# Performance work log

Measured on AMD Instinct MI355X. Metric: run time of the kernel, lower is better.

Reference implementation:

```python
import jax, jax.numpy as jnp
import numpy as np

B, L, S, H, C = 64, 512, 512, 768, 9  # batch, bert subword len, word seq len, hidden, num_classes


def setup_inputs() -> dict:
    key = jax.random.key(0)
    k1, k2, k3 = jax.random.split(key, 3)
    rng = np.random.RandomState(0)
    # per-word subword counts in {1,2,3}; truncate so totals fit in L subword slots
    lens = rng.randint(1, 4, size=(B, S))
    cum = lens.cumsum(axis=1)
    keep = cum <= L
    ids_lens = (lens * keep).astype(np.int32)
    totals = ids_lens.sum(axis=1)
    attention_mask = (np.arange(L)[None, :] < totals[:, None]).astype(np.int32)
    label_mask = ids_lens > 0
    label_ids = (rng.randint(0, C, size=(B, S)) * label_mask).astype(np.int32)
    bert_out = jax.random.normal(k1, (B, L, H), dtype=jnp.float32)
    W = jax.random.normal(k2, (H, C), dtype=jnp.float32) * 0.02
    b = jnp.zeros((C,), dtype=jnp.float32)
    return {
        "bert_out": bert_out,
        "W": W,
        "b": b,
        "attention_mask": jnp.asarray(attention_mask),
        "ids_lens": jnp.asarray(ids_lens),
        "label_ids": jnp.asarray(label_ids),
        "label_mask": jnp.asarray(label_mask),
    }


def reference(bert_out, W, b, attention_mask, ids_lens, label_ids, label_mask):
    Bv, Lv, Hv = bert_out.shape
    Sv = ids_lens.shape[1]
    nseg = Bv * Sv
    am = attention_mask.astype(jnp.int32)
    # subword position within each example's valid region
    sidx = jnp.cumsum(am, axis=1) - 1                       # [B, L]
    # word index for each subword: searchsorted into cumulative word lengths
    ends = jnp.cumsum(ids_lens, axis=1)                     # [B, S]
    widx = jax.vmap(lambda e, s: jnp.searchsorted(e, s, side='right'))(ends, sidx)
    seg = jnp.where(am > 0, widx + jnp.arange(Bv)[:, None] * Sv, nseg)  # pad bucket = nseg
    flat = bert_out.reshape(Bv * Lv, Hv)
    segf = seg.reshape(Bv * Lv)
    sums = jax.ops.segment_sum(flat, segf, num_segments=nseg + 1)[:nseg]
    cnts = jax.ops.segment_sum(jnp.ones((Bv * Lv,), bert_out.dtype), segf,
                               num_segments=nseg + 1)[:nseg]
    mean = sums / jnp.maximum(cnts, 1.0)[:, None]           # segment mean (split().mean(0))
    word_mask = (ids_lens > 0).reshape(nseg)
    embed = jnp.where(word_mask[:, None], mean, 0.0).reshape(Bv, Sv, Hv)  # masked_scatter
    # dropout in eval mode = identity
    logits = embed @ W + b                                  # [B, S, C]
    logp = jax.nn.log_softmax(logits, axis=-1)
    lab = jnp.clip(label_ids, 0, W.shape[1] - 1)
    nll = -jnp.take_along_axis(logp, lab[..., None].astype(jnp.int32), axis=-1)[..., 0]
    valid = label_mask.astype(bert_out.dtype)
    loss = jnp.sum(nll * valid) / jnp.maximum(jnp.sum(valid), 1.0)
    pred = jnp.argmax(logits, axis=-1)
    return loss, pred
```

## Files before the change

kernel.cpp:

```cpp
#include <hip/hip_runtime.h>

#define BB 64
#define LL 512
#define SS 512
#define HH 768
#define CC 9
#define NROWS (BB * LL)
#define RLS 12
#define G1 1024
#define ROWS_PER_BLOCK 32
#define WPS 64
#define G2 (BB * SS / WPS)

template <int CTRL>
__device__ __forceinline__ float dpp_add(float x) {
    int y = __builtin_amdgcn_update_dpp(0, __float_as_int(x), CTRL, 0xf, 0xf, true);
    return x + __int_as_float(y);
}
__device__ __forceinline__ float rsum64(float x) {
    x = dpp_add<0x111>(x);
    x = dpp_add<0x112>(x);
    x = dpp_add<0x114>(x);
    x = dpp_add<0x118>(x);
    x = dpp_add<0x142>(x);
    x = dpp_add<0x143>(x);
    return x;
}

__global__ __launch_bounds__(256) void wt_kernel(const float* __restrict__ Wm,
                                                 float* __restrict__ WT_g) {
    int e = blockIdx.x * 256 + threadIdx.x;
    if (e < HH * CC) {
        int h = e / CC;
        int c = e - h * CC;
        WT_g[c * HH + h] = Wm[e];
    }
}

__global__ __launch_bounds__(256) void row_gemm_kernel(
    const float* __restrict__ bert,
    const float* __restrict__ WT_g,
    float* __restrict__ RL)
{
    int wave = threadIdx.x >> 6;
    int lane = threadIdx.x & 63;
    int hoff = lane * 4;

    float4 wreg[CC][3];
#pragma unroll
    for (int c = 0; c < CC; c++)
#pragma unroll
        for (int c3 = 0; c3 < 3; c3++)
            wreg[c][c3] = *reinterpret_cast<const float4*>(WT_g + c * HH + c3 * 256 + hoff);

    size_t row0 = (size_t)blockIdx.x * ROWS_PER_BLOCK + wave * 8;

#pragma unroll
    for (int r = 0; r < 8; ++r) {
        const float* p = bert + (row0 + r) * HH + hoff;
        float4 f0 = *reinterpret_cast<const float4*>(p);
        float4 f1 = *reinterpret_cast<const float4*>(p + 256);
        float4 f2 = *reinterpret_cast<const float4*>(p + 512);

        float acc[CC];
#pragma unroll
        for (int c = 0; c < CC; c++) {
            acc[c] = f0.x * wreg[c][0].x + f0.y * wreg[c][0].y
                   + f0.z * wreg[c][0].z + f0.w * wreg[c][0].w
                   + f1.x * wreg[c][1].x + f1.y * wreg[c][1].y
                   + f1.z * wreg[c][1].z + f1.w * wreg[c][1].w
                   + f2.x * wreg[c][2].x + f2.y * wreg[c][2].y
                   + f2.z * wreg[c][2].z + f2.w * wreg[c][2].w;
        }
#pragma unroll
        for (int c = 0; c < CC; c++) acc[c] = rsum64(acc[c]);

        if (lane == 63) {
            float* dst = RL + (row0 + r) * RLS;
            float4 s0; s0.x = acc[0]; s0.y = acc[1]; s0.z = acc[2]; s0.w = acc[3];
            float4 s1; s1.x = acc[4]; s1.y = acc[5]; s1.z = acc[6]; s1.w = acc[7];
            *reinterpret_cast<float4*>(dst) = s0;
            *reinterpret_cast<float4*>(dst + 4) = s1;
            dst[8] = acc[8];
        }
    }
}

__global__ __launch_bounds__(256) void pool_kernel(
    const float* __restrict__ RL,
    const float* __restrict__ bias,
    const int* __restrict__ ids_lens,
    const int* __restrict__ label_ids,
    float* __restrict__ pred_out,
    float* __restrict__ nll_part,
    float* __restrict__ cnt_part)
{
    __shared__ int wlen[WPS], woff[WPS];
    __shared__ float red[4];
    __shared__ int s_start;

    int b = blockIdx.x >> 3;
    int s8 = blockIdx.x & 7;
    int w0 = s8 * WPS;
    const int* lens = ids_lens + b * SS;

    int t = threadIdx.x, lane = t & 63, wave = t >> 6;

    if (t < WPS) wlen[t] = lens[w0 + t];

    int part = 0;
    for (int i = t; i < w0; i += 256) part += lens[i];
    float pf = rsum64((float)part);
    if (lane == 63) red[wave] = pf;
    __syncthreads();
    if (t == 0) {
        int run = 0;
#pragma unroll
        for (int k = 0; k < WPS; k++) { woff[k] = run; run += wlen[k]; }
        s_start = (int)(red[0] + red[1] + red[2] + red[3]);
    }
    __syncthreads();

    if (t < 64) {
        int k = t;
        int len = wlen[k];
        int off = s_start + woff[k];
        const float* base = RL + ((size_t)b * LL + off) * RLS;

        float s[CC];
#pragma unroll
        for (int c = 0; c < CC; c++) s[c] = 0.0f;
        for (int j = 0; j < len; ++j) {
            const float* p = base + j * RLS;
            float4 a = *reinterpret_cast<const float4*>(p);
            float4 c4 = *reinterpret_cast<const float4*>(p + 4);
            s[0] += a.x;  s[1] += a.y;  s[2] += a.z;  s[3] += a.w;
            s[4] += c4.x; s[5] += c4.y; s[6] += c4.z; s[7] += c4.w;
            s[8] += p[8];
        }
        float inv = 1.0f / (float)(len > 0 ? len : 1);
        float lg[CC];
#pragma unroll
        for (int c = 0; c < CC; c++) lg[c] = s[c] * inv + bias[c];

        float mx = lg[0];
        int arg = 0;
#pragma unroll
        for (int c = 1; c < CC; c++) {
            if (lg[c] > mx) { mx = lg[c]; arg = c; }
        }
        float se = 0.0f;
#pragma unroll
        for (int c = 0; c < CC; c++) se += expf(lg[c] - mx);
        float lse = mx + logf(se);

        int g = b * SS + w0 + k;
        int lab = label_ids[g];
        lab = lab < 0 ? 0 : (lab > CC - 1 ? CC - 1 : lab);
        float valid = (len > 0) ? 1.0f : 0.0f;
        float nll = (lse - lg[lab]) * valid;

        pred_out[g] = (float)arg;

        float rn = rsum64(nll);
        float rc = rsum64(valid);
        if (t == 63) {
            nll_part[blockIdx.x] = rn;
            cnt_part[blockIdx.x] = rc;
        }
    }
}

__global__ __launch_bounds__(512) void finalize_kernel(
    const float* __restrict__ nll_part,
    const float* __restrict__ cnt_part,
    float* __restrict__ out_loss) {
    __shared__ float sn[8], sc[8];
    int t = threadIdx.x, lane = t & 63, wave = t >> 6;
    float n = rsum64(nll_part[t]);
    float c = rsum64(cnt_part[t]);
    if (lane == 63) { sn[wave] = n; sc[wave] = c; }
    __syncthreads();
    if (t == 0) {
        float tn = 0.0f, tc = 0.0f;
#pragma unroll
        for (int i = 0; i < 8; i++) { tn += sn[i]; tc += sc[i]; }
        out_loss[0] = tn / fmaxf(tc, 1.0f);
    }
}

extern "C" void kernel_launch(void* const* d_in, const int* in_sizes, int n_in,
                              void* d_out, int out_size, void* d_ws, size_t ws_size,
                              hipStream_t stream) {
    const float* bert = (const float*)d_in[0];
    const float* Wm   = (const float*)d_in[1];
    const float* bias = (const float*)d_in[2];
    const int* ids_lens  = (const int*)d_in[4];
    const int* label_ids = (const int*)d_in[5];

    float* out = (float*)d_out;

    float* WT_g     = (float*)d_ws;
    float* RL       = WT_g + CC * HH;
    float* nll_part = RL + (size_t)NROWS * RLS;
    float* cnt_part = nll_part + G2;

    wt_kernel<<<(HH * CC + 255) / 256, 256, 0, stream>>>(Wm, WT_g);
    row_gemm_kernel<<<G1, 256, 0, stream>>>(bert, WT_g, RL);
    pool_kernel<<<G2, 256, 0, stream>>>(RL, bias, ids_lens, label_ids,
                                        out + 1, nll_part, cnt_part);
    finalize_kernel<<<1, 512, 0, stream>>>(nll_part, cnt_part, out);
}
```

Baseline: 168.4 us.

## Precompute word offsets in setup kernel, fuse finalize into pool via atomic counter

Folds the W transpose and a per-batch prefix scan of ids_lens into one setup kernel, so the pool kernel reads word start offsets directly instead of recomputing partial sums per block. The pool kernel shrinks to 64 threads per block, and the last block to finish, detected with an atomic counter, computes the final loss, which removes the separate finalize launch. The row GEMM now processes two rows per iteration for more memory-level parallelism. This adds threadfence/atomic ordering and extra workspace for starts and the counter.

After: 176.2 us. 4.6% more time.

```diff
diff --git a/kernel.cpp b/kernel.cpp
--- a/kernel.cpp
+++ b/kernel.cpp
@@ -8,7 +8,6 @@
 #define NROWS (BB * LL)
 #define RLS 12
 #define G1 1024
-#define ROWS_PER_BLOCK 32
 #define WPS 64
 #define G2 (BB * SS / WPS)
 
@@ -27,13 +26,33 @@
     return x;
 }
 
-__global__ __launch_bounds__(256) void wt_kernel(const float* __restrict__ Wm,
-                                                 float* __restrict__ WT_g) {
-    int e = blockIdx.x * 256 + threadIdx.x;
-    if (e < HH * CC) {
-        int h = e / CC;
-        int c = e - h * CC;
-        WT_g[c * HH + h] = Wm[e];
+__global__ __launch_bounds__(512) void setup_kernel(
+    const float* __restrict__ Wm,
+    const int* __restrict__ ids_lens,
+    int* __restrict__ starts,
+    float* __restrict__ WT_g,
+    int* __restrict__ done) {
+    __shared__ int buf[SS];
+    int blk = blockIdx.x, t = threadIdx.x;
+    if (blk < BB) {
+        int v = ids_lens[blk * SS + t];
+        buf[t] = v;
+        __syncthreads();
+        for (int off = 1; off < SS; off <<= 1) {
+            int x = (t >= off) ? buf[t - off] : 0;
+            __syncthreads();
+            buf[t] += x;
+            __syncthreads();
+        }
+        starts[blk * SS + t] = buf[t] - v;
+        if (blk == 0 && t == 0) *done = 0;
+    } else {
+        int e = (blk - BB) * 512 + t;
+        if (e < HH * CC) {
+            int h = e / CC;
+            int c = e - h * CC;
+            WT_g[c * HH + h] = Wm[e];
+        }
     }
 }
 
@@ -53,139 +72,134 @@
         for (int c3 = 0; c3 < 3; c3++)
             wreg[c][c3] = *reinterpret_cast<const float4*>(WT_g + c * HH + c3 * 256 + hoff);
 
-    size_t row0 = (size_t)blockIdx.x * ROWS_PER_BLOCK + wave * 8;
-
-#pragma unroll
-    for (int r = 0; r < 8; ++r) {
-        const float* p = bert + (row0 + r) * HH + hoff;
-        float4 f0 = *reinterpret_cast<const float4*>(p);
-        float4 f1 = *reinterpret_cast<const float4*>(p + 256);
-        float4 f2 = *reinterpret_cast<const float4*>(p + 512);
-
-        float acc[CC];
+    size_t row0 = (size_t)blockIdx.x * 32 + wave * 8;
+
+#pragma unroll
+    for (int rp = 0; rp < 4; ++rp) {
+        const float* pa = bert + (row0 + 2 * rp) * HH + hoff;
+        const float* pb = pa + HH;
+        float4 a0 = *reinterpret_cast<const float4*>(pa);
+        float4 a1 = *reinterpret_cast<const float4*>(pa + 256);
+        float4 a2 = *reinterpret_cast<const float4*>(pa + 512);
+        float4 b0 = *reinterpret_cast<const float4*>(pb);
+        float4 b1 = *reinterpret_cast<const float4*>(pb + 256);
+        float4 b2 = *reinterpret_cast<const float4*>(pb + 512);
+
+        float acca[CC], accb[CC];
 #pragma unroll
         for (int c = 0; c < CC; c++) {
-            acc[c] = f0.x * wreg[c][0].x + f0.y * wreg[c][0].y
-                   + f0.z * wreg[c][0].z + f0.w * wreg[c][0].w
-                   + f1.x * wreg[c][1].x + f1.y * wreg[c][1].y
-                   + f1.z * wreg[c][1].z + f1.w * wreg[c][1].w
-                   + f2.x * wreg[c][2].x + f2.y * wreg[c][2].y
-                   + f2.z * wreg[c][2].z + f2.w * wreg[c][2].w;
-        }
-#pragma unroll
-        for (int c = 0; c < CC; c++) acc[c] = rsum64(acc[c]);
+            acca[c] = a0.x * wreg[c][0].x + a0.y * wreg[c][0].y
+                    + a0.z * wreg[c][0].z + a0.w * wreg[c][0].w
+                    + a1.x * wreg[c][1].x + a1.y * wreg[c][1].y
+                    + a1.z * wreg[c][1].z + a1.w * wreg[c][1].w
+                    + a2.x * wreg[c][2].x + a2.y * wreg[c][2].y
+                    + a2.z * wreg[c][2].z + a2.w * wreg[c][2].w;
+            accb[c] = b0.x * wreg[c][0].x + b0.y * wreg[c][0].y
+                    + b0.z * wreg[c][0].z + b0.w * wreg[c][0].w
+                    + b1.x * wreg[c][1].x + b1.y * wreg[c][1].y
+                    + b1.z * wreg[c][1].z + b1.w * wreg[c][1].w
+                    + b2.x * wreg[c][2].x + b2.y * wreg[c][2].y
+                    + b2.z * wreg[c][2].z + b2.w * wreg[c][2].w;
+        }
+#pragma unroll
+        for (int c = 0; c < CC; c++) { acca[c] = rsum64(acca[c]); accb[c] = rsum64(accb[c]); }
 
         if (lane == 63) {
-            float* dst = RL + (row0 + r) * RLS;
-            float4 s0; s0.x = acc[0]; s0.y = acc[1]; s0.z = acc[2]; s0.w = acc[3];
-            float4 s1; s1.x = acc[4]; s1.y = acc[5]; s1.z = acc[6]; s1.w = acc[7];
-            *reinterpret_cast<float4*>(dst) = s0;
-            *reinterpret_cast<float4*>(dst + 4) = s1;
-            dst[8] = acc[8];
-        }
-    }
-}
-
-__global__ __launch_bounds__(256) void pool_kernel(
+            float* da = RL + (row0 + 2 * rp) * RLS;
+            float* db = da + RLS;
+            float4 s0, s1;
+            s0.x = acca[0]; s0.y = acca[1]; s0.z = acca[2]; s0.w = acca[3];
+            s1.x = acca[4]; s1.y = acca[5]; s1.z = acca[6]; s1.w = acca[7];
+            *reinterpret_cast<float4*>(da) = s0;
+            *reinterpret_cast<float4*>(da + 4) = s1;
+            da[8] = acca[8];
+            s0.x = accb[0]; s0.y = accb[1]; s0.z = accb[2]; s0.w = accb[3];
+            s1.x = accb[4]; s1.y = accb[5]; s1.z = accb[6]; s1.w = accb[7];
+            *reinterpret_cast<float4*>(db) = s0;
+            *reinterpret_cast<float4*>(db + 4) = s1;
+            db[8] = accb[8];
+        }
+    }
+}
+
+__global__ __launch_bounds__(64) void pool_kernel(
     const float* __restrict__ RL,
     const float* __restrict__ bias,
     const int* __restrict__ ids_lens,
     const int* __restrict__ label_ids,
+    const int* __restrict__ starts,
     float* __restrict__ pred_out,
     float* __restrict__ nll_part,
-    float* __restrict__ cnt_part)
+    float* __restrict__ cnt_part,
+    int* __restrict__ done,
+    float* __restrict__ out_loss)
 {
-    __shared__ int wlen[WPS], woff[WPS];
-    __shared__ float red[4];
-    __shared__ int s_start;
-
+    __shared__ int s_old;
     int b = blockIdx.x >> 3;
     int s8 = blockIdx.x & 7;
-    int w0 = s8 * WPS;
-    const int* lens = ids_lens + b * SS;
-
-    int t = threadIdx.x, lane = t & 63, wave = t >> 6;
-
-    if (t < WPS) wlen[t] = lens[w0 + t];
-
-    int part = 0;
-    for (int i = t; i < w0; i += 256) part += lens[i];
-    float pf = rsum64((float)part);
-    if (lane == 63) red[wave] = pf;
+    int k = threadIdx.x;
+    int g = b * SS + s8 * WPS + k;
+
+    int len = ids_lens[g];
+    int off = starts[g];
+    const float* base = RL + ((size_t)b * LL + off) * RLS;
+
+    float s[CC];
+#pragma unroll
+    for (int c = 0; c < CC; c++) s[c] = 0.0f;
+    for (int j = 0; j < len; ++j) {
+        const float* p = base + j * RLS;
+        float4 a = *reinterpret_cast<const float4*>(p);
+        float4 c4 = *reinterpret_cast<const float4*>(p + 4);
+        s[0] += a.x;  s[1] += a.y;  s[2] += a.z;  s[3] += a.w;
+        s[4] += c4.x; s[5] += c4.y; s[6] += c4.z; s[7] += c4.w;
+        s[8] += p[8];
+    }
+    float inv = 1.0f / (float)(len > 0 ? len : 1);
+    float lg[CC];
+#pragma unroll
+    for (int c = 0; c < CC; c++) lg[c] = s[c] * inv + bias[c];
+
+    float mx = lg[0];
+    int arg = 0;
+#pragma unroll
+    for (int c = 1; c < CC; c++) {
+        if (lg[c] > mx) { mx = lg[c]; arg = c; }
+    }
+    float se = 0.0f;
+#pragma unroll
+    for (int c = 0; c < CC; c++) se += expf(lg[c] - mx);
+    float lse = mx + logf(se);
+
+    int lab = label_ids[g];
+    lab = lab < 0 ? 0 : (lab > CC - 1 ? CC - 1 : lab);
+    float valid = (len > 0) ? 1.0f : 0.0f;
+    float nll = (lse - lg[lab]) * valid;
+
+    pred_out[g] = (float)arg;
+
+    float rn = rsum64(nll);
+    float rc = rsum64(valid);
+    if (k == 63) {
+        nll_part[blockIdx.x] = rn;
+        cnt_part[blockIdx.x] = rc;
+    }
+    __threadfence();
     __syncthreads();
-    if (t == 0) {
-        int run = 0;
-#pragma unroll
-        for (int k = 0; k < WPS; k++) { woff[k] = run; run += wlen[k]; }
-        s_start = (int)(red[0] + red[1] + red[2] + red[3]);
-    }
+    if (k == 0) s_old = atomicAdd(done, 1);
     __syncthreads();
 
-    if (t < 64) {
-        int k = t;
-        int len = wlen[k];
-        int off = s_start + woff[k];
-        const float* base = RL + ((size_t)b * LL + off) * RLS;
-
-        float s[CC];
-#pragma unroll
-        for (int c = 0; c < CC; c++) s[c] = 0.0f;
-        for (int j = 0; j < len; ++j) {
-            const float* p = base + j * RLS;
-            float4 a = *reinterpret_cast<const float4*>(p);
-            float4 c4 = *reinterpret_cast<const float4*>(p + 4);
-            s[0] += a.x;  s[1] += a.y;  s[2] += a.z;  s[3] += a.w;
-            s[4] += c4.x; s[5] += c4.y; s[6] += c4.z; s[7] += c4.w;
-            s[8] += p[8];
-        }
-        float inv = 1.0f / (float)(len > 0 ? len : 1);
-        float lg[CC];
-#pragma unroll
-        for (int c = 0; c < CC; c++) lg[c] = s[c] * inv + bias[c];
-
-        float mx = lg[0];
-        int arg = 0;
-#pragma unroll
-        for (int c = 1; c < CC; c++) {
-            if (lg[c] > mx) { mx = lg[c]; arg = c; }
-        }
-        float se = 0.0f;
-#pragma unroll
-        for (int c = 0; c < CC; c++) se += expf(lg[c] - mx);
-        float lse = mx + logf(se);
-
-        int g = b * SS + w0 + k;
-        int lab = label_ids[g];
-        lab = lab < 0 ? 0 : (lab > CC - 1 ? CC - 1 : lab);
-        float valid = (len > 0) ? 1.0f : 0.0f;
-        float nll = (lse - lg[lab]) * valid;
-
-        pred_out[g] = (float)arg;
-
-        float rn = rsum64(nll);
-        float rc = rsum64(valid);
-        if (t == 63) {
-            nll_part[blockIdx.x] = rn;
-            cnt_part[blockIdx.x] = rc;
-        }
-    }
-}
-
-__global__ __launch_bounds__(512) void finalize_kernel(
-    const float* __restrict__ nll_part,
-    const float* __restrict__ cnt_part,
-    float* __restrict__ out_loss) {
-    __shared__ float sn[8], sc[8];
-    int t = threadIdx.x, lane = t & 63, wave = t >> 6;
-    float n = rsum64(nll_part[t]);
-    float c = rsum64(cnt_part[t]);
-    if (lane == 63) { sn[wave] = n; sc[wave] = c; }
-    __syncthreads();
-    if (t == 0) {
-        float tn = 0.0f, tc = 0.0f;
-#pragma unroll
-        for (int i = 0; i < 8; i++) { tn += sn[i]; tc += sc[i]; }
-        out_loss[0] = tn / fmaxf(tc, 1.0f);
+    if (s_old == G2 - 1) {
+        __threadfence();
+        float n = 0.0f, c = 0.0f;
+#pragma unroll
+        for (int i = 0; i < G2 / 64; i++) {
+            n += nll_part[k + 64 * i];
+            c += cnt_part[k + 64 * i];
+        }
+        n = rsum64(n);
+        c = rsum64(c);
+        if (k == 63) out_loss[0] = n / fmaxf(c, 1.0f);
     }
 }
 
@@ -204,10 +218,12 @@
     float* RL       = WT_g + CC * HH;
     float* nll_part = RL + (size_t)NROWS * RLS;
     float* cnt_part = nll_part + G2;
-
-    wt_kernel<<<(HH * CC + 255) / 256, 256, 0, stream>>>(Wm, WT_g);
+    int*   starts   = (int*)(cnt_part + G2);
+    int*   done     = starts + BB * SS;
+
+    setup_kernel<<<BB + (HH * CC + 511) / 512, 512, 0, stream>>>(Wm, ids_lens,
+                                                                 starts, WT_g, done);
     row_gemm_kernel<<<G1, 256, 0, stream>>>(bert, WT_g, RL);
-    pool_kernel<<<G2, 256, 0, stream>>>(RL, bias, ids_lens, label_ids,
-                                        out + 1, nll_part, cnt_part);
-    finalize_kernel<<<1, 512, 0, stream>>>(nll_part, cnt_part, out);
-}
+    pool_kernel<<<G2, 64, 0, stream>>>(RL, bias, ids_lens, label_ids, starts,
+                                       out + 1, nll_part, cnt_part, done, out);
+}
```

## Split classes across waves in row GEMM to cut register pressure

Applied to the files above, without the earlier changes.

Row GEMM blocks now have three waves, each computing three of the nine class logits for the same 16 rows, instead of each wave computing all nine classes for its own 8 rows. This reduces the per-thread weight registers from 27 float4 to 9, allowing higher occupancy. All three waves now load the same bert row data, relying on cache hits, and a mid-loop barrier keeps them in step. The risk is extra cache traffic from the repeated loads and the barrier cost.

New measurement: 169.5 us. No clear change (+0.6%).

```diff
diff --git a/kernel.cpp b/kernel.cpp
--- a/kernel.cpp
+++ b/kernel.cpp
@@ -7,8 +7,8 @@
 #define CC 9
 #define NROWS (BB * LL)
 #define RLS 12
-#define G1 1024
-#define ROWS_PER_BLOCK 32
+#define RPB 16
+#define G1 (NROWS / RPB)
 #define WPS 64
 #define G2 (BB * SS / WPS)
 
@@ -37,7 +37,7 @@
     }
 }
 
-__global__ __launch_bounds__(256) void row_gemm_kernel(
+__global__ __launch_bounds__(192) void row_gemm_kernel(
     const float* __restrict__ bert,
     const float* __restrict__ WT_g,
     float* __restrict__ RL)
@@ -45,26 +45,29 @@
     int wave = threadIdx.x >> 6;
     int lane = threadIdx.x & 63;
     int hoff = lane * 4;
-
-    float4 wreg[CC][3];
-#pragma unroll
-    for (int c = 0; c < CC; c++)
+    int c0 = wave * 3;
+
+    float4 wreg[3][3];
+#pragma unroll
+    for (int c = 0; c < 3; c++)
 #pragma unroll
         for (int c3 = 0; c3 < 3; c3++)
-            wreg[c][c3] = *reinterpret_cast<const float4*>(WT_g + c * HH + c3 * 256 + hoff);
-
-    size_t row0 = (size_t)blockIdx.x * ROWS_PER_BLOCK + wave * 8;
-
-#pragma unroll
-    for (int r = 0; r < 8; ++r) {
+            wreg[c][c3] = *reinterpret_cast<const float4*>(
+                WT_g + (c0 + c) * HH + c3 * 256 + hoff);
+
+    size_t row0 = (size_t)blockIdx.x * RPB;
+
+#pragma unroll
+    for (int r = 0; r < RPB; ++r) {
+        if (r == RPB / 2) __syncthreads();
         const float* p = bert + (row0 + r) * HH + hoff;
         float4 f0 = *reinterpret_cast<const float4*>(p);
         float4 f1 = *reinterpret_cast<const float4*>(p + 256);
         float4 f2 = *reinterpret_cast<const float4*>(p + 512);
 
-        float acc[CC];
-#pragma unroll
-        for (int c = 0; c < CC; c++) {
+        float acc[3];
+#pragma unroll
+        for (int c = 0; c < 3; c++) {
             acc[c] = f0.x * wreg[c][0].x + f0.y * wreg[c][0].y
                    + f0.z * wreg[c][0].z + f0.w * wreg[c][0].w
                    + f1.x * wreg[c][1].x + f1.y * wreg[c][1].y
@@ -73,15 +76,13 @@
                    + f2.z * wreg[c][2].z + f2.w * wreg[c][2].w;
         }
 #pragma unroll
-        for (int c = 0; c < CC; c++) acc[c] = rsum64(acc[c]);
+        for (int c = 0; c < 3; c++) acc[c] = rsum64(acc[c]);
 
         if (lane == 63) {
-            float* dst = RL + (row0 + r) * RLS;
-            float4 s0; s0.x = acc[0]; s0.y = acc[1]; s0.z = acc[2]; s0.w = acc[3];
-            float4 s1; s1.x = acc[4]; s1.y = acc[5]; s1.z = acc[6]; s1.w = acc[7];
-            *reinterpret_cast<float4*>(dst) = s0;
-            *reinterpret_cast<float4*>(dst + 4) = s1;
-            dst[8] = acc[8];
+            float* dst = RL + (row0 + r) * RLS + c0;
+            dst[0] = acc[0];
+            dst[1] = acc[1];
+            dst[2] = acc[2];
         }
     }
 }
@@ -206,7 +207,7 @@
     float* cnt_part = nll_part + G2;
 
     wt_kernel<<<(HH * CC + 255) / 256, 256, 0, stream>>>(Wm, WT_g);
-    row_gemm_kernel<<<G1, 256, 0, stream>>>(bert, WT_g, RL);
+    row_gemm_kernel<<<G1, 192, 0, stream>>>(bert, WT_g, RL);
     pool_kernel<<<G2, 256, 0, stream>>>(RL, bias, ids_lens, label_ids,
                                         out + 1, nll_part, cnt_part);
     finalize_kernel<<<1, 512, 0, stream>>>(nll_part, cnt_part, out);
```
